# Kernel optimization log

Measured on AMD Instinct MI355X. Metric: run time of the kernel, lower is better.

The kernel has to match this reference:

```python
import jax, jax.numpy as jnp
import numpy as np

S, B, H = 512, 64, 1024


def setup_inputs() -> dict:
    key = jax.random.key(0)
    ks = jax.random.split(key, 9)
    sc = 1.0 / np.sqrt(2 * H)
    return {
        "hidden": jax.random.normal(ks[0], (B, H), jnp.float32),
        "decoder_out": jax.random.normal(ks[1], (B, H), jnp.float32),
        "encoder_states": jax.random.normal(ks[2], (S, B, H), jnp.float32),
        "W_attn": jax.random.uniform(ks[3], (2 * H, 2 * H), jnp.float32, -sc, sc),
        "b_attn": jax.random.uniform(ks[4], (2 * H,), jnp.float32, -sc, sc),
        "W_attn2": jax.random.uniform(ks[5], (1, 2 * H), jnp.float32, -sc, sc),
        "b_attn2": jax.random.uniform(ks[6], (1,), jnp.float32, -sc, sc),
        "W_comb": jax.random.uniform(ks[7], (H, 2 * H), jnp.float32, -sc, sc),
        "b_comb": jax.random.uniform(ks[8], (H,), jnp.float32, -sc, sc),
    }


def reference(hidden, decoder_out, encoder_states, W_attn, b_attn, W_attn2, b_attn2, W_comb, b_comb):
    s, b, h = encoder_states.shape
    # per-timestep cat(hidden, enc_t) -> attn -> tanh -> attn2, fully batched over S
    hid = jnp.broadcast_to(hidden[None], (s, b, h))
    cat = jnp.concatenate([hid, encoder_states], axis=-1)            # [S,B,2H]
    scores = jnp.tanh(cat @ W_attn.T + b_attn) @ W_attn2.T + b_attn2  # [S,B,1]
    scores = scores[..., 0].T                                         # [B,S] (stack dim=1 + squeeze)
    attn_w = jax.nn.softmax(scores, axis=-1)                          # [B,S]
    # bmm([B,1,S], [B,S,H]) -> [B,H]
    applied = jnp.einsum("bs,sbh->bh", attn_w, encoder_states)
    out = jnp.concatenate([decoder_out, applied], axis=-1) @ W_comb.T + b_comb
    out = jnp.tanh(out)
    return out, applied
```

## Files before the change

### kernel.cpp

```cpp
#include <hip/hip_runtime.h>
#include <stdint.h>


typedef __attribute__((ext_vector_type(8))) short bf16x8;
typedef __attribute__((ext_vector_type(4))) float f32x4;

__device__ __forceinline__ float bf2f(uint16_t u) {
  return __uint_as_float(((uint32_t)u) << 16);
}
__device__ __forceinline__ uint16_t f2bf(float x) {
  uint32_t u = __float_as_uint(x);
  u += 0x7fffu + ((u >> 16) & 1u);
  return (uint16_t)(u >> 16);
}
__device__ __forceinline__ uint32_t pk2(float a, float b) {
  return (uint32_t)f2bf(a) | ((uint32_t)f2bf(b) << 16);
}
__device__ __forceinline__ uint4 cvt8(const float* __restrict__ p) {
  const float4 a = *(const float4*)p;
  const float4 b = *(const float4*)(p + 4);
  uint4 r;
  r.x = pk2(a.x, a.y); r.y = pk2(a.z, a.w);
  r.z = pk2(b.x, b.y); r.w = pk2(b.z, b.w);
  return r;
}
__device__ __forceinline__ float tanh_fast(float x) {
  const float e = __expf(2.f * x);
  return __builtin_fmaf(-2.f, __builtin_amdgcn_rcpf(e + 1.f), 1.f);
}
__device__ __forceinline__ void load16(const uint16_t* g, uint16_t* l) {
  __builtin_amdgcn_global_load_lds(
      (const __attribute__((address_space(1))) void*)g,
      (__attribute__((address_space(3))) void*)l, 16, 0, 0);
}

__global__ __launch_bounds__(256)
void cvt_all_kernel(const float* __restrict__ enc, const float* __restrict__ Wa,
                    const float* __restrict__ Wc,
                    uint16_t* __restrict__ enc_bf, uint16_t* __restrict__ Wa_bf,
                    uint16_t* __restrict__ Wc_bf,
                    float* __restrict__ scores, float* __restrict__ U,
                    const float* __restrict__ ba) {
  const int tid0 = blockIdx.x * 256 + threadIdx.x;
  if (tid0 < 32768) {
    scores[tid0] = 0.f;
#pragma unroll
    for (int k = 0; k < 4; ++k) {
      const int i = tid0 * 4 + k;
      U[i] = ba[i & 2047];
    }
  }
  const int stride = gridDim.x * 256;
  for (int idx = tid0; idx < 4718592; idx += stride) {
    if (idx < 4194304) {
      ((uint4*)enc_bf)[idx] = cvt8(enc + (size_t)idx * 8);
    } else if (idx < 4456448) {
      const int k = idx - 4194304;
      const int j = k >> 7, c8 = k & 127;
      ((uint4*)Wa_bf)[k] = cvt8(Wa + (size_t)j * 2048 + 1024 + c8 * 8);
    } else {
      const int k = idx - 4456448;
      ((uint4*)Wc_bf)[k] = cvt8(Wc + (size_t)k * 8);
    }
  }
}

__global__ __launch_bounds__(256)
void gemm_u_kernel(const float* __restrict__ A, const float* __restrict__ B32,
                   float* __restrict__ U) {
  __shared__ __align__(16) uint16_t sA[128 * 32];
  __shared__ __align__(16) uint16_t sB[128 * 32];
  const int t = threadIdx.x, lane = t & 63, wave = t >> 6;
  const int wm = wave >> 1, wn = wave & 1;
  const int bn0 = blockIdx.x * 128;
  const int kbase = blockIdx.y * 256;
  const int srow = t >> 2, scol = (t & 3) * 8;
  const int ar0 = min(srow, 63), ar1 = min(64 + srow, 63);
  f32x4 acc[4][4];
#pragma unroll
  for (int i = 0; i < 4; ++i)
#pragma unroll
    for (int j = 0; j < 4; ++j) acc[i][j] = (f32x4){0.f, 0.f, 0.f, 0.f};
  const int mrow = wm * 64 + (lane & 15);
  const int nrow = wn * 64 + (lane & 15);
  const int kq = (lane >> 4) * 8;
  for (int kk = 0; kk < 8; ++kk) {
    const int k0 = kbase + (kk << 5);
    const uint4 va0 = cvt8(A + (size_t)ar0 * 1024 + scol + k0);
    const uint4 va1 = cvt8(A + (size_t)ar1 * 1024 + scol + k0);
    const uint4 vb0 = cvt8(B32 + (size_t)(bn0 + srow) * 2048 + scol + k0);
    const uint4 vb1 = cvt8(B32 + (size_t)(bn0 + 64 + srow) * 2048 + scol + k0);
    __syncthreads();
    *(uint4*)&sA[t * 8] = va0;
    *(uint4*)&sA[2048 + t * 8] = va1;
    *(uint4*)&sB[t * 8] = vb0;
    *(uint4*)&sB[2048 + t * 8] = vb1;
    __syncthreads();
    bf16x8 af[4], bfr[4];
#pragma unroll
    for (int i = 0; i < 4; ++i) af[i] = *(const bf16x8*)&sA[(mrow + i * 16) * 32 + kq];
#pragma unroll
    for (int j = 0; j < 4; ++j) bfr[j] = *(const bf16x8*)&sB[(nrow + j * 16) * 32 + kq];
#pragma unroll
    for (int i = 0; i < 4; ++i)
#pragma unroll
      for (int j = 0; j < 4; ++j)
        acc[i][j] = __builtin_amdgcn_mfma_f32_16x16x32_bf16(af[i], bfr[j], acc[i][j], 0, 0, 0);
  }
  const int colb = lane & 15, rquad = lane >> 4;
#pragma unroll
  for (int i = 0; i < 4; ++i)
#pragma unroll
    for (int r = 0; r < 4; ++r) {
      const int gm = wm * 64 + i * 16 + rquad * 4 + r;
      if (gm < 64) {
#pragma unroll
        for (int j = 0; j < 4; ++j) {
          const int gn = bn0 + wn * 64 + j * 16 + colb;
          atomicAdd(&U[gm * 2048 + gn], acc[i][j][r]);
        }
      }
    }
}

template <int MODE, int NT>
__global__ __launch_bounds__(256)
void gemm_bf_kernel(const uint16_t* __restrict__ A, int lda,
                    const uint16_t* __restrict__ Bm, int ldb,
                    int M, float* __restrict__ outf,
                    const float* __restrict__ Ubias,
                    const float* __restrict__ bias) {
  __shared__ __align__(16) uint16_t lds[3][2][4096];

  const int t = threadIdx.x, lane = t & 63, wave = t >> 6;
  const int wm = wave >> 1, wn = wave & 1;
  int bm0, bn0, kbase;
  if (MODE == 1) {
    const int wid = blockIdx.x;
    const int xcd = wid & 7, q = wid >> 3;
    bm0 = (xcd * 32 + (q >> 4)) * 128;
    bn0 = (q & 15) * 128;
    kbase = 0;
  } else {
    bm0 = 0;
    bn0 = blockIdx.y * 128;
    kbase = blockIdx.z * (NT * 32);
  }

  const uint16_t* gpA[2];
  const uint16_t* gpB[2];
  int sb[2];
#pragma unroll
  for (int q = 0; q < 2; ++q) {
    const int s = q * 256 + t;
    const int r = s >> 2, kc = s & 3;
    const int g = kc ^ ((r >> 1) & 3);
    gpA[q] = A + (size_t)min(bm0 + r, M - 1) * lda + kbase + g * 8;
    gpB[q] = Bm + (size_t)(bn0 + r) * ldb + kbase + g * 8;
    sb[q] = (q * 256 + wave * 64) * 8;
  }

  f32x4 acc[4][4];
#pragma unroll
  for (int i = 0; i < 4; ++i)
#pragma unroll
    for (int j = 0; j < 4; ++j) acc[i][j] = (f32x4){0.f, 0.f, 0.f, 0.f};

  const int swz = ((lane >> 1) & 3) << 3;
  const int kq = ((lane >> 4) * 8) ^ swz;
  const int aoff = (wm * 64 + (lane & 15)) * 32 + kq;
  const int boff = (wn * 64 + (lane & 15)) * 32 + kq;

#pragma unroll
  for (int q = 0; q < 2; ++q) {
    load16(gpA[q], &lds[0][0][sb[q]]);
    load16(gpB[q], &lds[0][1][sb[q]]);
  }
#pragma unroll
  for (int q = 0; q < 2; ++q) {
    load16(gpA[q] + 32, &lds[1][0][sb[q]]);
    load16(gpB[q] + 32, &lds[1][1][sb[q]]);
  }
  asm volatile("s_waitcnt vmcnt(4)" ::: "memory");
  __builtin_amdgcn_s_barrier();

#pragma unroll
  for (int kt = 0; kt < NT; ++kt) {
    const int bufc = kt % 3;
    if (kt + 2 < NT) {
      const int nb = (kt + 2) % 3;
      const int kpre = (kt + 2) * 32;
#pragma unroll
      for (int q = 0; q < 2; ++q) {
        load16(gpA[q] + kpre, &lds[nb][0][sb[q]]);
        load16(gpB[q] + kpre, &lds[nb][1][sb[q]]);
      }
    }
    const uint16_t* sA = lds[bufc][0];
    const uint16_t* sB = lds[bufc][1];
    bf16x8 af[4], bfr[4];
#pragma unroll
    for (int i = 0; i < 4; ++i) af[i] = *(const bf16x8*)&sA[aoff + i * 512];
#pragma unroll
    for (int j = 0; j < 4; ++j) bfr[j] = *(const bf16x8*)&sB[boff + j * 512];
#pragma unroll
    for (int i = 0; i < 4; ++i)
#pragma unroll
      for (int j = 0; j < 4; ++j)
        acc[i][j] = __builtin_amdgcn_mfma_f32_16x16x32_bf16(af[i], bfr[j], acc[i][j], 0, 0, 0);
    if (kt + 2 < NT) {
      asm volatile("s_waitcnt vmcnt(4) lgkmcnt(0)" ::: "memory");
      __builtin_amdgcn_s_barrier();
    } else if (kt + 1 < NT) {
      asm volatile("s_waitcnt vmcnt(0) lgkmcnt(0)" ::: "memory");
      __builtin_amdgcn_s_barrier();
    }
  }

  const int colb = lane & 15, rquad = lane >> 4;
  if (MODE == 1) {
    float w2f[4];
#pragma unroll
    for (int j = 0; j < 4; ++j) w2f[j] = bias[bn0 + wn * 64 + j * 16 + colb];
#pragma unroll
    for (int i = 0; i < 4; ++i) {
#pragma unroll
      for (int r = 0; r < 4; ++r) {
        const int gm = bm0 + wm * 64 + i * 16 + rquad * 4 + r;
        const int bb = gm & 63;
        float p = 0.f;
#pragma unroll
        for (int j = 0; j < 4; ++j) {
          const float u = Ubias[bb * 2048 + bn0 + wn * 64 + j * 16 + colb];
          p += tanh_fast(acc[i][j][r] + u) * w2f[j];
        }
        p += __shfl_xor(p, 1);
        p += __shfl_xor(p, 2);
        p += __shfl_xor(p, 4);
        p += __shfl_xor(p, 8);
        if (colb == 0) atomicAdd(outf + gm, p);
      }
    }
  } else {
    const float bsc = (blockIdx.z == 0) ? 1.f : 0.f;
#pragma unroll
    for (int i = 0; i < 4; ++i)
#pragma unroll
      for (int r = 0; r < 4; ++r) {
        const int gm = bm0 + wm * 64 + i * 16 + rquad * 4 + r;
        if (gm < M) {
#pragma unroll
          for (int j = 0; j < 4; ++j) {
            const int gn = bn0 + wn * 64 + j * 16 + colb;
            atomicAdd(outf + gm * 1024 + gn, acc[i][j][r] + bsc * bias[gn]);
          }
        }
      }
  }
}

__global__ __launch_bounds__(256)
void applied_kernel(const uint16_t* __restrict__ encb, const float* __restrict__ dec,
                    const float* __restrict__ scores,
                    float* __restrict__ out_applied, uint16_t* __restrict__ acat,
                    float* __restrict__ out_acc) {
  const int b = blockIdx.x, chunk = blockIdx.y, t = threadIdx.x;
  const int wave = t >> 6, lane = t & 63;
  __shared__ float w[512];
  __shared__ float red[8];
  __shared__ float2 part2[256];
  float v0 = scores[(size_t)t * 64 + b];
  float v1 = scores[(size_t)(t + 256) * 64 + b];
  float mx = fmaxf(v0, v1);
#pragma unroll
  for (int off = 32; off >= 1; off >>= 1) mx = fmaxf(mx, __shfl_xor(mx, off));
  if (lane == 0) red[wave] = mx;
  __syncthreads();
  mx = fmaxf(fmaxf(red[0], red[1]), fmaxf(red[2], red[3]));
  const float e0 = __expf(v0 - mx), e1 = __expf(v1 - mx);
  float sum = e0 + e1;
#pragma unroll
  for (int off = 32; off >= 1; off >>= 1) sum += __shfl_xor(sum, off);
  if (lane == 0) red[4 + wave] = sum;
  __syncthreads();
  sum = (red[4] + red[5]) + (red[6] + red[7]);
  const float inv = 1.f / sum;
  w[t] = e0 * inv;
  w[t + 256] = e1 * inv;
  __syncthreads();
  const int hp = t & 31, sq = t >> 5;
  const int h = chunk * 64 + hp * 2;
  const uint32_t* base = (const uint32_t*)encb + (size_t)b * 512 + (h >> 1);
  float a0 = 0.f, a1 = 0.f;
#pragma unroll 8
  for (int s = sq * 64; s < sq * 64 + 64; ++s) {
    const uint32_t p = base[(size_t)s * 32768];
    a0 += w[s] * bf2f((uint16_t)(p & 0xffffu));
    a1 += w[s] * bf2f((uint16_t)(p >> 16));
  }
  part2[t] = make_float2(a0, a1);
  __syncthreads();
  if (t < 32) {
    a0 = 0.f; a1 = 0.f;
#pragma unroll
    for (int k = 0; k < 8; ++k) {
      const float2 pp = part2[t + 32 * k];
      a0 += pp.x; a1 += pp.y;
    }
    *(float2*)(out_applied + (size_t)b * 1024 + h) = make_float2(a0, a1);
    *(uint32_t*)(acat + (size_t)b * 2048 + 1024 + h) = pk2(a0, a1);
    *(uint32_t*)(acat + (size_t)b * 2048 + h) =
        pk2(dec[(size_t)b * 1024 + h], dec[(size_t)b * 1024 + h + 1]);
    *(float2*)(out_acc + (size_t)b * 1024 + h) = make_float2(0.f, 0.f);
  }
}

__global__ __launch_bounds__(256)
void tanh_kernel(const float* __restrict__ acc, float* __restrict__ outp) {
  const int i = blockIdx.x * 256 + threadIdx.x;
  float4 v = ((const float4*)acc)[i];
  v.x = tanh_fast(v.x); v.y = tanh_fast(v.y);
  v.z = tanh_fast(v.z); v.w = tanh_fast(v.w);
  ((float4*)outp)[i] = v;
}

extern "C" void kernel_launch(void* const* d_in, const int* in_sizes, int n_in,
                              void* d_out, int out_size, void* d_ws, size_t ws_size,
                              hipStream_t stream) {
  const float* hidden  = (const float*)d_in[0];
  const float* dec     = (const float*)d_in[1];
  const float* enc     = (const float*)d_in[2];
  const float* W_attn  = (const float*)d_in[3];
  const float* b_attn  = (const float*)d_in[4];
  const float* W_attn2 = (const float*)d_in[5];
  const float* W_comb  = (const float*)d_in[7];
  const float* b_comb  = (const float*)d_in[8];
  float* outp = (float*)d_out;

  char* ws = (char*)d_ws;
  float*    scores = (float*)(ws + 0);
  float*    U      = (float*)(ws + 131072);
  float*    out_acc= (float*)(ws + 131072);
  uint16_t* acat   = (uint16_t*)(ws + 655360);
  uint16_t* enc_bf = (uint16_t*)(ws + 1048576);
  uint16_t* Wa_bf  = (uint16_t*)(ws + 68157440);
  uint16_t* Wc_bf  = (uint16_t*)(ws + 72351744);

  cvt_all_kernel<<<4608, 256, 0, stream>>>(enc, W_attn, W_comb, enc_bf, Wa_bf,
                                           Wc_bf, scores, U, b_attn);
  gemm_u_kernel<<<dim3(16, 4), 256, 0, stream>>>(hidden, W_attn, U);
  gemm_bf_kernel<1, 32><<<4096, 256, 0, stream>>>(
      enc_bf, 1024, Wa_bf, 1024, 32768, scores, U, W_attn2);
  applied_kernel<<<dim3(64, 16), 256, 0, stream>>>(enc_bf, dec, scores,
                                                   outp + 65536, acat, out_acc);
  gemm_bf_kernel<3, 16><<<dim3(1, 8, 4), 256, 0, stream>>>(
      acat, 2048, Wc_bf, 2048, 64, out_acc, nullptr, b_comb);
  tanh_kernel<<<64, 256, 0, stream>>>(out_acc, outp);
}
```

Baseline: 456.9 us.

## Enlarge score GEMM tiles to 256x256 with 512-thread blocks

Measured after the change: 451.8 us. No clear change (-1.1%).

```diff
diff --git a/kernel.cpp b/kernel.cpp
--- a/kernel.cpp
+++ b/kernel.cpp
@@ -123,67 +123,59 @@
     }
 }
 
-template <int MODE, int NT>
-__global__ __launch_bounds__(256)
-void gemm_bf_kernel(const uint16_t* __restrict__ A, int lda,
-                    const uint16_t* __restrict__ Bm, int ldb,
-                    int M, float* __restrict__ outf,
-                    const float* __restrict__ Ubias,
-                    const float* __restrict__ bias) {
-  __shared__ __align__(16) uint16_t lds[3][2][4096];
+__global__ __launch_bounds__(512, 2)
+void gemm_score_kernel(const uint16_t* __restrict__ A,
+                       const uint16_t* __restrict__ Bm,
+                       float* __restrict__ outf,
+                       const float* __restrict__ Ubias,
+                       const float* __restrict__ bias) {
+  __shared__ __align__(16) uint16_t lds[3][2][8192];
 
   const int t = threadIdx.x, lane = t & 63, wave = t >> 6;
-  const int wm = wave >> 1, wn = wave & 1;
-  int bm0, bn0, kbase;
-  if (MODE == 1) {
-    const int wid = blockIdx.x;
-    const int xcd = wid & 7, q = wid >> 3;
-    bm0 = (xcd * 32 + (q >> 4)) * 128;
-    bn0 = (q & 15) * 128;
-    kbase = 0;
-  } else {
-    bm0 = 0;
-    bn0 = blockIdx.y * 128;
-    kbase = blockIdx.z * (NT * 32);
-  }
+  const int wm = wave >> 2, wn = wave & 3;
+  const int wid = blockIdx.x;
+  const int xcd = wid & 7, q = wid >> 3;
+  const int bm0 = (xcd * 16 + (q >> 3)) * 256;
+  const int bn0 = (q & 7) * 256;
 
   const uint16_t* gpA[2];
   const uint16_t* gpB[2];
   int sb[2];
 #pragma unroll
-  for (int q = 0; q < 2; ++q) {
-    const int s = q * 256 + t;
+  for (int qq = 0; qq < 2; ++qq) {
+    const int s = qq * 512 + t;
     const int r = s >> 2, kc = s & 3;
     const int g = kc ^ ((r >> 1) & 3);
-    gpA[q] = A + (size_t)min(bm0 + r, M - 1) * lda + kbase + g * 8;
-    gpB[q] = Bm + (size_t)(bn0 + r) * ldb + kbase + g * 8;
-    sb[q] = (q * 256 + wave * 64) * 8;
-  }
-
-  f32x4 acc[4][4];
-#pragma unroll
-  for (int i = 0; i < 4; ++i)
+    gpA[qq] = A + (size_t)(bm0 + r) * 1024 + g * 8;
+    gpB[qq] = Bm + (size_t)(bn0 + r) * 1024 + g * 8;
+    sb[qq] = (qq * 512 + wave * 64) * 8;
+  }
+
+  f32x4 acc[8][4];
+#pragma unroll
+  for (int i = 0; i < 8; ++i)
 #pragma unroll
     for (int j = 0; j < 4; ++j) acc[i][j] = (f32x4){0.f, 0.f, 0.f, 0.f};
 
   const int swz = ((lane >> 1) & 3) << 3;
   const int kq = ((lane >> 4) * 8) ^ swz;
-  const int aoff = (wm * 64 + (lane & 15)) * 32 + kq;
+  const int aoff = (wm * 128 + (lane & 15)) * 32 + kq;
   const int boff = (wn * 64 + (lane & 15)) * 32 + kq;
 
 #pragma unroll
-  for (int q = 0; q < 2; ++q) {
-    load16(gpA[q], &lds[0][0][sb[q]]);
-    load16(gpB[q], &lds[0][1][sb[q]]);
-  }
-#pragma unroll
-  for (int q = 0; q < 2; ++q) {
-    load16(gpA[q] + 32, &lds[1][0][sb[q]]);
-    load16(gpB[q] + 32, &lds[1][1][sb[q]]);
+  for (int qq = 0; qq < 2; ++qq) {
+    load16(gpA[qq], &lds[0][0][sb[qq]]);
+    load16(gpB[qq], &lds[0][1][sb[qq]]);
+  }
+#pragma unroll
+  for (int qq = 0; qq < 2; ++qq) {
+    load16(gpA[qq] + 32, &lds[1][0][sb[qq]]);
+    load16(gpB[qq] + 32, &lds[1][1][sb[qq]]);
   }
   asm volatile("s_waitcnt vmcnt(4)" ::: "memory");
   __builtin_amdgcn_s_barrier();
 
+  constexpr int NT = 32;
 #pragma unroll
   for (int kt = 0; kt < NT; ++kt) {
     const int bufc = kt % 3;
@@ -191,20 +183,20 @@
       const int nb = (kt + 2) % 3;
       const int kpre = (kt + 2) * 32;
 #pragma unroll
-      for (int q = 0; q < 2; ++q) {
-        load16(gpA[q] + kpre, &lds[nb][0][sb[q]]);
-        load16(gpB[q] + kpre, &lds[nb][1][sb[q]]);
+      for (int qq = 0; qq < 2; ++qq) {
+        load16(gpA[qq] + kpre, &lds[nb][0][sb[qq]]);
+        load16(gpB[qq] + kpre, &lds[nb][1][sb[qq]]);
       }
     }
     const uint16_t* sA = lds[bufc][0];
     const uint16_t* sB = lds[bufc][1];
-    bf16x8 af[4], bfr[4];
-#pragma unroll
-    for (int i = 0; i < 4; ++i) af[i] = *(const bf16x8*)&sA[aoff + i * 512];
+    bf16x8 af[8], bfr[4];
+#pragma unroll
+    for (int i = 0; i < 8; ++i) af[i] = *(const bf16x8*)&sA[aoff + i * 512];
 #pragma unroll
     for (int j = 0; j < 4; ++j) bfr[j] = *(const bf16x8*)&sB[boff + j * 512];
 #pragma unroll
-    for (int i = 0; i < 4; ++i)
+    for (int i = 0; i < 8; ++i)
 #pragma unroll
       for (int j = 0; j < 4; ++j)
         acc[i][j] = __builtin_amdgcn_mfma_f32_16x16x32_bf16(af[i], bfr[j], acc[i][j], 0, 0, 0);
@@ -218,45 +210,129 @@
   }
 
   const int colb = lane & 15, rquad = lane >> 4;
-  if (MODE == 1) {
-    float w2f[4];
-#pragma unroll
-    for (int j = 0; j < 4; ++j) w2f[j] = bias[bn0 + wn * 64 + j * 16 + colb];
-#pragma unroll
-    for (int i = 0; i < 4; ++i) {
-#pragma unroll
-      for (int r = 0; r < 4; ++r) {
-        const int gm = bm0 + wm * 64 + i * 16 + rquad * 4 + r;
-        const int bb = gm & 63;
-        float p = 0.f;
+  float w2f[4];
+#pragma unroll
+  for (int j = 0; j < 4; ++j) w2f[j] = bias[bn0 + wn * 64 + j * 16 + colb];
+#pragma unroll
+  for (int i = 0; i < 8; ++i) {
+#pragma unroll
+    for (int r = 0; r < 4; ++r) {
+      const int gm = bm0 + wm * 128 + i * 16 + rquad * 4 + r;
+      const int bb = gm & 63;
+      float p = 0.f;
+#pragma unroll
+      for (int j = 0; j < 4; ++j) {
+        const float u = Ubias[bb * 2048 + bn0 + wn * 64 + j * 16 + colb];
+        p += tanh_fast(acc[i][j][r] + u) * w2f[j];
+      }
+      p += __shfl_xor(p, 1);
+      p += __shfl_xor(p, 2);
+      p += __shfl_xor(p, 4);
+      p += __shfl_xor(p, 8);
+      if (colb == 0) atomicAdd(outf + gm, p);
+    }
+  }
+}
+
+template <int NT>
+__global__ __launch_bounds__(256)
+void gemm_comb_kernel(const uint16_t* __restrict__ A, int lda,
+                      const uint16_t* __restrict__ Bm, int ldb,
+                      int M, float* __restrict__ outf,
+                      const float* __restrict__ bias) {
+  __shared__ __align__(16) uint16_t lds[3][2][4096];
+
+  const int t = threadIdx.x, lane = t & 63, wave = t >> 6;
+  const int wm = wave >> 1, wn = wave & 1;
+  const int bm0 = 0;
+  const int bn0 = blockIdx.y * 128;
+  const int kbase = blockIdx.z * (NT * 32);
+
+  const uint16_t* gpA[2];
+  const uint16_t* gpB[2];
+  int sb[2];
+#pragma unroll
+  for (int q = 0; q < 2; ++q) {
+    const int s = q * 256 + t;
+    const int r = s >> 2, kc = s & 3;
+    const int g = kc ^ ((r >> 1) & 3);
+    gpA[q] = A + (size_t)min(bm0 + r, M - 1) * lda + kbase + g * 8;
+    gpB[q] = Bm + (size_t)(bn0 + r) * ldb + kbase + g * 8;
+    sb[q] = (q * 256 + wave * 64) * 8;
+  }
+
+  f32x4 acc[4][4];
+#pragma unroll
+  for (int i = 0; i < 4; ++i)
+#pragma unroll
+    for (int j = 0; j < 4; ++j) acc[i][j] = (f32x4){0.f, 0.f, 0.f, 0.f};
+
+  const int swz = ((lane >> 1) & 3) << 3;
+  const int kq = ((lane >> 4) * 8) ^ swz;
+  const int aoff = (wm * 64 + (lane & 15)) * 32 + kq;
+  const int boff = (wn * 64 + (lane & 15)) * 32 + kq;
+
+#pragma unroll
+  for (int q = 0; q < 2; ++q) {
+    load16(gpA[q], &lds[0][0][sb[q]]);
+    load16(gpB[q], &lds[0][1][sb[q]]);
+  }
+#pragma unroll
+  for (int q = 0; q < 2; ++q) {
+    load16(gpA[q] + 32, &lds[1][0][sb[q]]);
+    load16(gpB[q] + 32, &lds[1][1][sb[q]]);
+  }
+  asm volatile("s_waitcnt vmcnt(4)" ::: "memory");
+  __builtin_amdgcn_s_barrier();
+
+#pragma unroll
+  for (int kt = 0; kt < NT; ++kt) {
+    const int bufc = kt % 3;
+    if (kt + 2 < NT) {
+      const int nb = (kt + 2) % 3;
+      const int kpre = (kt + 2) * 32;
+#pragma unroll
+      for (int q = 0; q < 2; ++q) {
+        load16(gpA[q] + kpre, &lds[nb][0][sb[q]]);
+        load16(gpB[q] + kpre, &lds[nb][1][sb[q]]);
+      }
+    }
+    const uint16_t* sA = lds[bufc][0];
+    const uint16_t* sB = lds[bufc][1];
+    bf16x8 af[4], bfr[4];
+#pragma unroll
+    for (int i = 0; i < 4; ++i) af[i] = *(const bf16x8*)&sA[aoff + i * 512];
+#pragma unroll
+    for (int j = 0; j < 4; ++j) bfr[j] = *(const bf16x8*)&sB[boff + j * 512];
+#pragma unroll
+    for (int i = 0; i < 4; ++i)
+#pragma unroll
+      for (int j = 0; j < 4; ++j)
+        acc[i][j] = __builtin_amdgcn_mfma_f32_16x16x32_bf16(af[i], bfr[j], acc[i][j], 0, 0, 0);
+    if (kt + 2 < NT) {
+      asm volatile("s_waitcnt vmcnt(4) lgkmcnt(0)" ::: "memory");
+      __builtin_amdgcn_s_barrier();
+    } else if (kt + 1 < NT) {
+      asm volatile("s_waitcnt vmcnt(0) lgkmcnt(0)" ::: "memory");
+      __builtin_amdgcn_s_barrier();
+    }
+  }
+
+  const int colb = lane & 15, rquad = lane >> 4;
+  const float bsc = (blockIdx.z == 0) ? 1.f : 0.f;
+#pragma unroll
+  for (int i = 0; i < 4; ++i)
+#pragma unroll
+    for (int r = 0; r < 4; ++r) {
+      const int gm = bm0 + wm * 64 + i * 16 + rquad * 4 + r;
+      if (gm < M) {
 #pragma unroll
         for (int j = 0; j < 4; ++j) {
-          const float u = Ubias[bb * 2048 + bn0 + wn * 64 + j * 16 + colb];
-          p += tanh_fast(acc[i][j][r] + u) * w2f[j];
-        }
-        p += __shfl_xor(p, 1);
-        p += __shfl_xor(p, 2);
-        p += __shfl_xor(p, 4);
-        p += __shfl_xor(p, 8);
-        if (colb == 0) atomicAdd(outf + gm, p);
-      }
-    }
-  } else {
-    const float bsc = (blockIdx.z == 0) ? 1.f : 0.f;
-#pragma unroll
-    for (int i = 0; i < 4; ++i)
-#pragma unroll
-      for (int r = 0; r < 4; ++r) {
-        const int gm = bm0 + wm * 64 + i * 16 + rquad * 4 + r;
-        if (gm < M) {
-#pragma unroll
-          for (int j = 0; j < 4; ++j) {
-            const int gn = bn0 + wn * 64 + j * 16 + colb;
-            atomicAdd(outf + gm * 1024 + gn, acc[i][j][r] + bsc * bias[gn]);
-          }
+          const int gn = bn0 + wn * 64 + j * 16 + colb;
+          atomicAdd(outf + gm * 1024 + gn, acc[i][j][r] + bsc * bias[gn]);
         }
       }
-  }
+    }
 }
 
 __global__ __launch_bounds__(256)
@@ -349,11 +425,10 @@
   cvt_all_kernel<<<4608, 256, 0, stream>>>(enc, W_attn, W_comb, enc_bf, Wa_bf,
                                            Wc_bf, scores, U, b_attn);
   gemm_u_kernel<<<dim3(16, 4), 256, 0, stream>>>(hidden, W_attn, U);
-  gemm_bf_kernel<1, 32><<<4096, 256, 0, stream>>>(
-      enc_bf, 1024, Wa_bf, 1024, 32768, scores, U, W_attn2);
+  gemm_score_kernel<<<1024, 512, 0, stream>>>(enc_bf, Wa_bf, scores, U, W_attn2);
   applied_kernel<<<dim3(64, 16), 256, 0, stream>>>(enc_bf, dec, scores,
                                                    outp + 65536, acat, out_acc);
-  gemm_bf_kernel<3, 16><<<dim3(1, 8, 4), 256, 0, stream>>>(
-      acat, 2048, Wc_bf, 2048, 64, out_acc, nullptr, b_comb);
+  gemm_comb_kernel<16><<<dim3(1, 8, 4), 256, 0, stream>>>(
+      acat, 2048, Wc_bf, 2048, 64, out_acc, b_comb);
   tanh_kernel<<<64, 256, 0, stream>>>(out_acc, outp);
 }
```

## Widen score GEMM tiles to 128x256 and fuse comb GEMM with tanh

Applied to the files above, without the earlier changes.

After: 467.4 us. +2.3%, slower.

```diff
diff --git a/kernel.cpp b/kernel.cpp
--- a/kernel.cpp
+++ b/kernel.cpp
@@ -123,42 +123,34 @@
     }
 }
 
-template <int MODE, int NT>
-__global__ __launch_bounds__(256)
-void gemm_bf_kernel(const uint16_t* __restrict__ A, int lda,
-                    const uint16_t* __restrict__ Bm, int ldb,
-                    int M, float* __restrict__ outf,
-                    const float* __restrict__ Ubias,
-                    const float* __restrict__ bias) {
-  __shared__ __align__(16) uint16_t lds[3][2][4096];
+__global__ __launch_bounds__(512, 4)
+void gemm_score_kernel(const uint16_t* __restrict__ A,
+                       const uint16_t* __restrict__ Bm,
+                       float* __restrict__ outf,
+                       const float* __restrict__ Ubias,
+                       const float* __restrict__ bias) {
+  __shared__ __align__(16) uint16_t lds[2][12288];
 
   const int t = threadIdx.x, lane = t & 63, wave = t >> 6;
-  const int wm = wave >> 1, wn = wave & 1;
-  int bm0, bn0, kbase;
-  if (MODE == 1) {
-    const int wid = blockIdx.x;
-    const int xcd = wid & 7, q = wid >> 3;
-    bm0 = (xcd * 32 + (q >> 4)) * 128;
-    bn0 = (q & 15) * 128;
-    kbase = 0;
-  } else {
-    bm0 = 0;
-    bn0 = blockIdx.y * 128;
-    kbase = blockIdx.z * (NT * 32);
-  }
-
-  const uint16_t* gpA[2];
+  const int wm = wave >> 2, wn = wave & 3;
+  const int wid = blockIdx.x;
+  const int xcd = wid & 7, q = wid >> 3;
+  const int bm0 = (xcd * 32 + (q >> 3)) * 128;
+  const int bn0 = (q & 7) * 256;
+
+  const int rA = t >> 2, kcA = t & 3;
+  const uint16_t* gpA =
+      A + (size_t)(bm0 + rA) * 1024 + (kcA ^ ((rA >> 1) & 3)) * 8;
   const uint16_t* gpB[2];
-  int sb[2];
-#pragma unroll
-  for (int q = 0; q < 2; ++q) {
-    const int s = q * 256 + t;
-    const int r = s >> 2, kc = s & 3;
-    const int g = kc ^ ((r >> 1) & 3);
-    gpA[q] = A + (size_t)min(bm0 + r, M - 1) * lda + kbase + g * 8;
-    gpB[q] = Bm + (size_t)(bn0 + r) * ldb + kbase + g * 8;
-    sb[q] = (q * 256 + wave * 64) * 8;
-  }
+#pragma unroll
+  for (int qq = 0; qq < 2; ++qq) {
+    const int sl = qq * 512 + t;
+    const int r = sl >> 2, kc = sl & 3;
+    gpB[qq] = Bm + (size_t)(bn0 + r) * 1024 + (kc ^ ((r >> 1) & 3)) * 8;
+  }
+  const int sbA = wave * 512;
+  const int sbB0 = 4096 + wave * 512;
+  const int sbB1 = 4096 + 4096 + wave * 512;
 
   f32x4 acc[4][4];
 #pragma unroll
@@ -168,36 +160,26 @@
 
   const int swz = ((lane >> 1) & 3) << 3;
   const int kq = ((lane >> 4) * 8) ^ swz;
-  const int aoff = (wm * 64 + (lane & 15)) * 32 + kq;
-  const int boff = (wn * 64 + (lane & 15)) * 32 + kq;
-
-#pragma unroll
-  for (int q = 0; q < 2; ++q) {
-    load16(gpA[q], &lds[0][0][sb[q]]);
-    load16(gpB[q], &lds[0][1][sb[q]]);
-  }
-#pragma unroll
-  for (int q = 0; q < 2; ++q) {
-    load16(gpA[q] + 32, &lds[1][0][sb[q]]);
-    load16(gpB[q] + 32, &lds[1][1][sb[q]]);
-  }
-  asm volatile("s_waitcnt vmcnt(4)" ::: "memory");
-  __builtin_amdgcn_s_barrier();
-
-#pragma unroll
-  for (int kt = 0; kt < NT; ++kt) {
-    const int bufc = kt % 3;
-    if (kt + 2 < NT) {
-      const int nb = (kt + 2) % 3;
-      const int kpre = (kt + 2) * 32;
-#pragma unroll
-      for (int q = 0; q < 2; ++q) {
-        load16(gpA[q] + kpre, &lds[nb][0][sb[q]]);
-        load16(gpB[q] + kpre, &lds[nb][1][sb[q]]);
-      }
-    }
-    const uint16_t* sA = lds[bufc][0];
-    const uint16_t* sB = lds[bufc][1];
+  const int rl = lane & 15;
+  const int aoff = (wm * 64 + rl) * 32 + kq;
+  const int boff = (wn * 64 + rl) * 32 + kq;
+
+  load16(gpA, &lds[0][sbA]);
+  load16(gpB[0], &lds[0][sbB0]);
+  load16(gpB[1], &lds[0][sbB1]);
+  __syncthreads();
+
+#pragma unroll
+  for (int s = 0; s < 32; ++s) {
+    const int cb = s & 1;
+    if (s + 1 < 32) {
+      const int nb = cb ^ 1, ko = (s + 1) * 32;
+      load16(gpA + ko, &lds[nb][sbA]);
+      load16(gpB[0] + ko, &lds[nb][sbB0]);
+      load16(gpB[1] + ko, &lds[nb][sbB1]);
+    }
+    const uint16_t* sA = &lds[cb][0];
+    const uint16_t* sB = &lds[cb][4096];
     bf16x8 af[4], bfr[4];
 #pragma unroll
     for (int i = 0; i < 4; ++i) af[i] = *(const bf16x8*)&sA[aoff + i * 512];
@@ -208,62 +190,64 @@
 #pragma unroll
       for (int j = 0; j < 4; ++j)
         acc[i][j] = __builtin_amdgcn_mfma_f32_16x16x32_bf16(af[i], bfr[j], acc[i][j], 0, 0, 0);
-    if (kt + 2 < NT) {
-      asm volatile("s_waitcnt vmcnt(4) lgkmcnt(0)" ::: "memory");
-      __builtin_amdgcn_s_barrier();
-    } else if (kt + 1 < NT) {
-      asm volatile("s_waitcnt vmcnt(0) lgkmcnt(0)" ::: "memory");
-      __builtin_amdgcn_s_barrier();
-    }
+    __syncthreads();
   }
 
   const int colb = lane & 15, rquad = lane >> 4;
-  if (MODE == 1) {
-    float w2f[4];
-#pragma unroll
-    for (int j = 0; j < 4; ++j) w2f[j] = bias[bn0 + wn * 64 + j * 16 + colb];
-#pragma unroll
-    for (int i = 0; i < 4; ++i) {
-#pragma unroll
-      for (int r = 0; r < 4; ++r) {
-        const int gm = bm0 + wm * 64 + i * 16 + rquad * 4 + r;
-        const int bb = gm & 63;
-        float p = 0.f;
-#pragma unroll
-        for (int j = 0; j < 4; ++j) {
-          const float u = Ubias[bb * 2048 + bn0 + wn * 64 + j * 16 + colb];
-          p += tanh_fast(acc[i][j][r] + u) * w2f[j];
-        }
-        p += __shfl_xor(p, 1);
-        p += __shfl_xor(p, 2);
-        p += __shfl_xor(p, 4);
-        p += __shfl_xor(p, 8);
-        if (colb == 0) atomicAdd(outf + gm, p);
+  float w2f[4];
+#pragma unroll
+  for (int j = 0; j < 4; ++j) w2f[j] = bias[bn0 + wn * 64 + j * 16 + colb];
+#pragma unroll
+  for (int i = 0; i < 4; ++i) {
+#pragma unroll
+    for (int r = 0; r < 4; ++r) {
+      const int gm = bm0 + wm * 64 + i * 16 + rquad * 4 + r;
+      const int bb = gm & 63;
+      float p = 0.f;
+#pragma unroll
+      for (int j = 0; j < 4; ++j) {
+        const float u = Ubias[bb * 2048 + bn0 + wn * 64 + j * 16 + colb];
+        p += tanh_fast(acc[i][j][r] + u) * w2f[j];
       }
-    }
-  } else {
-    const float bsc = (blockIdx.z == 0) ? 1.f : 0.f;
-#pragma unroll
-    for (int i = 0; i < 4; ++i)
-#pragma unroll
-      for (int r = 0; r < 4; ++r) {
-        const int gm = bm0 + wm * 64 + i * 16 + rquad * 4 + r;
-        if (gm < M) {
-#pragma unroll
-          for (int j = 0; j < 4; ++j) {
-            const int gn = bn0 + wn * 64 + j * 16 + colb;
-            atomicAdd(outf + gm * 1024 + gn, acc[i][j][r] + bsc * bias[gn]);
-          }
-        }
-      }
-  }
+      p += __shfl_xor(p, 1);
+      p += __shfl_xor(p, 2);
+      p += __shfl_xor(p, 4);
+      p += __shfl_xor(p, 8);
+      if (colb == 0) atomicAdd(outf + gm, p);
+    }
+  }
+}
+
+__global__ __launch_bounds__(512)
+void gemm_comb_kernel(const uint16_t* __restrict__ A,
+                      const uint16_t* __restrict__ Bm,
+                      float* __restrict__ outp,
+                      const float* __restrict__ bias) {
+  const int t = threadIdx.x, lane = t & 63, wave = t >> 6;
+  const int g = blockIdx.x * 8 + wave;
+  const int m0 = (g >> 6) * 16, n0 = (g & 63) * 16;
+  const int rl = lane & 15, kq = (lane >> 4) * 8;
+  const uint16_t* ap = A + (size_t)(m0 + rl) * 2048 + kq;
+  const uint16_t* bp = Bm + (size_t)(n0 + rl) * 2048 + kq;
+  f32x4 acc = (f32x4){0.f, 0.f, 0.f, 0.f};
+#pragma unroll 8
+  for (int ks = 0; ks < 64; ++ks) {
+    const bf16x8 af = *(const bf16x8*)(ap + ks * 32);
+    const bf16x8 bf = *(const bf16x8*)(bp + ks * 32);
+    acc = __builtin_amdgcn_mfma_f32_16x16x32_bf16(af, bf, acc, 0, 0, 0);
+  }
+  const int gm = m0 + (lane >> 4) * 4;
+  const int gn = n0 + rl;
+  const float bj = bias[gn];
+#pragma unroll
+  for (int r = 0; r < 4; ++r)
+    outp[(gm + r) * 1024 + gn] = tanh_fast(acc[r] + bj);
 }
 
 __global__ __launch_bounds__(256)
 void applied_kernel(const uint16_t* __restrict__ encb, const float* __restrict__ dec,
                     const float* __restrict__ scores,
-                    float* __restrict__ out_applied, uint16_t* __restrict__ acat,
-                    float* __restrict__ out_acc) {
+                    float* __restrict__ out_applied, uint16_t* __restrict__ acat) {
   const int b = blockIdx.x, chunk = blockIdx.y, t = threadIdx.x;
   const int wave = t >> 6, lane = t & 63;
   __shared__ float w[512];
@@ -311,17 +295,7 @@
     *(uint32_t*)(acat + (size_t)b * 2048 + 1024 + h) = pk2(a0, a1);
     *(uint32_t*)(acat + (size_t)b * 2048 + h) =
         pk2(dec[(size_t)b * 1024 + h], dec[(size_t)b * 1024 + h + 1]);
-    *(float2*)(out_acc + (size_t)b * 1024 + h) = make_float2(0.f, 0.f);
-  }
-}
-
-__global__ __launch_bounds__(256)
-void tanh_kernel(const float* __restrict__ acc, float* __restrict__ outp) {
-  const int i = blockIdx.x * 256 + threadIdx.x;
-  float4 v = ((const float4*)acc)[i];
-  v.x = tanh_fast(v.x); v.y = tanh_fast(v.y);
-  v.z = tanh_fast(v.z); v.w = tanh_fast(v.w);
-  ((float4*)outp)[i] = v;
+  }
 }
 
 extern "C" void kernel_launch(void* const* d_in, const int* in_sizes, int n_in,
@@ -340,7 +314,6 @@
   char* ws = (char*)d_ws;
   float*    scores = (float*)(ws + 0);
   float*    U      = (float*)(ws + 131072);
-  float*    out_acc= (float*)(ws + 131072);
   uint16_t* acat   = (uint16_t*)(ws + 655360);
   uint16_t* enc_bf = (uint16_t*)(ws + 1048576);
   uint16_t* Wa_bf  = (uint16_t*)(ws + 68157440);
@@ -349,11 +322,8 @@
   cvt_all_kernel<<<4608, 256, 0, stream>>>(enc, W_attn, W_comb, enc_bf, Wa_bf,
                                            Wc_bf, scores, U, b_attn);
   gemm_u_kernel<<<dim3(16, 4), 256, 0, stream>>>(hidden, W_attn, U);
-  gemm_bf_kernel<1, 32><<<4096, 256, 0, stream>>>(
-      enc_bf, 1024, Wa_bf, 1024, 32768, scores, U, W_attn2);
+  gemm_score_kernel<<<2048, 512, 0, stream>>>(enc_bf, Wa_bf, scores, U, W_attn2);
   applied_kernel<<<dim3(64, 16), 256, 0, stream>>>(enc_bf, dec, scores,
-                                                   outp + 65536, acat, out_acc);
-  gemm_bf_kernel<3, 16><<<dim3(1, 8, 4), 256, 0, stream>>>(
-      acat, 2048, Wc_bf, 2048, 64, out_acc, nullptr, b_comb);
-  tanh_kernel<<<64, 256, 0, stream>>>(out_acc, outp);
-}
+                                                   outp + 65536, acat);
+  gemm_comb_kernel<<<32, 512, 0, stream>>>(acat, Wc_bf, outp, b_comb);
+}
```
